# Kernel tuning notes

Hardware: AMD Instinct MI355X
Metric: run time of the kernel (lower is better)

The kernel has to match this reference:

```python
import jax, jax.numpy as jnp
import numpy as np

B, N = 64, 8192
DEPTH, C_IN, C = 12, 4, 128


def _conv1x1(x, W, b):
    # x: [B, Cin, N], W: [Cout, Cin], b: [Cout] -> [B, Cout, N]
    return jnp.einsum('oc,bcn->bon', W, x) + b[None, :, None]


def setup_inputs() -> dict:
    key = jax.random.key(0)
    ks = jax.random.split(key, 10)
    s = 0.05
    return {
        'correspondence': jax.random.normal(ks[0], (B, C_IN, 1, N), jnp.float32),
        'W_first': jax.random.normal(ks[1], (C, C_IN), jnp.float32) * s,
        'b_first': jnp.zeros((C,), jnp.float32),
        'W1s': jax.random.normal(ks[2], (DEPTH, C, C), jnp.float32) * s,
        'b1s': jnp.zeros((DEPTH, C), jnp.float32),
        'W2s': jax.random.normal(ks[3], (DEPTH, C, C), jnp.float32) * s,
        'b2s': jnp.zeros((DEPTH, C), jnp.float32),
        'W_final': jax.random.normal(ks[4], (1, C), jnp.float32) * s,
        'b_final': jnp.zeros((1,), jnp.float32),
    }


def _forward(correspondence, W_first, b_first, W1s, b1s, W2s, b2s, W_final, b_final):
    x_in = correspondence                      # [B, 4, 1, N]
    xc = x_in[:, :, 0, :]                      # [B, 4, N]
    # weightNet: first conv, resnet blocks, final conv (all 1x1)
    h = _conv1x1(xc, W_first, b_first)         # [B, C, N]

    def block(h, p):
        W1, b1, W2, b2 = p
        y = jax.nn.relu(_conv1x1(h, W1, b1))
        y = _conv1x1(y, W2, b2)
        return jax.nn.relu(h + y), None

    h, _ = jax.lax.scan(block, h, (W1s, b1s, W2s, b2s))
    logits = _conv1x1(h, W_final, b_final)[:, 0, :]   # [B, N]
    weight = jax.nn.relu(jnp.tanh(logits))            # [B, N]

    xx = jnp.transpose(xc, (0, 2, 1))                 # [B, N, 4] = [x1, x2, y1, y2]
    x1, x2, y1, y2 = xx[..., 0], xx[..., 1], xx[..., 2], xx[..., 3]
    ones = jnp.ones_like(x1)
    # X: [B, N, 9] epipolar monomials
    X = jnp.stack([y1 * x1, y1 * x2, y1,
                   y2 * x1, y2 * x2, y2,
                   x1, x2, ones], axis=-1)
    # weighted normal matrix per sample: [B, 9, 9]
    XwX = jnp.einsum('bni,bn,bnj->bij', X, weight, X)
    # batched symmetric eigendecomposition; eigh sorts ascending -> min eigvec at index 0
    _, evecs = jnp.linalg.eigh(XwX)
    v = evecs[:, :, 0]                                # [B, 9]
    essential = v / jnp.linalg.norm(v, axis=1, keepdims=True)
    return essential


def reference(correspondence, W_first, b_first, W1s, b1s, W2s, b2s, W_final, b_final):
    return _forward(correspondence, W_first, b_first, W1s, b1s, W2s, b2s, W_final, b_final)
```

## Files before the change

kernel.cpp:

```cpp
#include <hip/hip_runtime.h>
#include <math.h>

#define NPTS 8192
#define CHN 128
#define NLAYER 12
#define LDH 136

typedef __attribute__((ext_vector_type(8))) _Float16 f16x8;
typedef __attribute__((ext_vector_type(4))) float f32x4;

__device__ inline void split_f16(float x, _Float16* hi, _Float16* lo) {
  _Float16 h = (_Float16)x;
  *hi = h;
  *lo = (_Float16)(x - (float)h);
}

union U2h { unsigned int u; _Float16 f[2]; };
union U4h { uint2 u; _Float16 f[4]; };

__global__ void prep_w_kernel(const float* __restrict__ W1s,
                              const float* __restrict__ W2s,
                              _Float16* __restrict__ Whi,
                              _Float16* __restrict__ Wlo) {
  int idx = blockIdx.x * 256 + threadIdx.x;
  if (idx >= 24 * 128 * 128) return;
  int conv = idx >> 14;
  int r = idx & 16383;
  const float* src = (conv & 1) ? (W2s + ((size_t)(conv >> 1) << 14))
                                : (W1s + ((size_t)(conv >> 1) << 14));
  _Float16 h, l;
  split_f16(src[r], &h, &l);
  Whi[idx] = h;
  Wlo[idx] = l;
}

__global__ __launch_bounds__(512, 6) void mlp_xwx_kernel(
    const float* __restrict__ xc,
    const float* __restrict__ Wfirst,
    const float* __restrict__ bfirst,
    const _Float16* __restrict__ Whi,
    const _Float16* __restrict__ Wlo,
    const float* __restrict__ b1s,
    const float* __restrict__ b2s,
    const float* __restrict__ Wfinal,
    const float* __restrict__ bfinal,
    float* __restrict__ partial) {
  __shared__ __align__(16) _Float16 Hh[64 * LDH];
  __shared__ __align__(16) _Float16 Yh[64 * LDH];
  __shared__ float red[8][64];
  const int tid = threadIdx.x;
  const int lane = tid & 63;
  const int wv = tid >> 6;
  const int l16 = lane & 15;
  const int quad = lane >> 4;
  const int o0 = wv << 4;
  const int b = blockIdx.x >> 7;
  const int n0 = (blockIdx.x & 127) << 6;

  const float* xb = xc + ((size_t)b * 4) * NPTS + n0 + lane;
  const float x1 = xb[0 * NPTS];
  const float x2 = xb[1 * NPTS];
  const float y1 = xb[2 * NPTS];
  const float y2 = xb[3 * NPTS];

  {
    #pragma unroll
    for (int j = 0; j < 16; j += 2) {
      int c = o0 + j;
      float h0 = bfirst[c] + Wfirst[c * 4 + 0] * x1 + Wfirst[c * 4 + 1] * x2 +
                 Wfirst[c * 4 + 2] * y1 + Wfirst[c * 4 + 3] * y2;
      float h1 = bfirst[c + 1] + Wfirst[(c + 1) * 4 + 0] * x1 + Wfirst[(c + 1) * 4 + 1] * x2 +
                 Wfirst[(c + 1) * 4 + 2] * y1 + Wfirst[(c + 1) * 4 + 3] * y2;
      U2h ph;
      ph.f[0] = (_Float16)h0;
      ph.f[1] = (_Float16)h1;
      *(unsigned int*)&Hh[lane * LDH + c] = ph.u;
    }
  }
  __syncthreads();

  const size_t arow = (size_t)(o0 + l16) * CHN + (size_t)quad * 8;

  for (int layer = 0; layer < NLAYER; ++layer) {
    {
      const _Float16* W1h = Whi + ((size_t)(2 * layer) << 14);
      const float* b1 = b1s + layer * CHN;
      f16x8 ah[4];
      #pragma unroll
      for (int kt = 0; kt < 4; ++kt)
        ah[kt] = *(const f16x8*)(W1h + arow + kt * 32);
      f32x4 acc[4];
      #pragma unroll
      for (int r = 0; r < 4; ++r) {
        float bv = b1[o0 + quad * 4 + r];
        #pragma unroll
        for (int nt = 0; nt < 4; ++nt) acc[nt][r] = bv;
      }
      #pragma unroll
      for (int kt = 0; kt < 4; ++kt) {
        #pragma unroll
        for (int nt = 0; nt < 4; ++nt) {
          f16x8 bh = *(const f16x8*)&Hh[(nt * 16 + l16) * LDH + kt * 32 + quad * 8];
          acc[nt] = __builtin_amdgcn_mfma_f32_16x16x32_f16(ah[kt], bh, acc[nt], 0, 0, 0);
        }
      }
      #pragma unroll
      for (int nt = 0; nt < 4; ++nt) {
        int p = nt * 16 + l16;
        int c = o0 + quad * 4;
        U4h ph;
        #pragma unroll
        for (int r = 0; r < 4; ++r)
          ph.f[r] = (_Float16)fmaxf(acc[nt][r], 0.0f);
        *(uint2*)&Yh[p * LDH + c] = ph.u;
      }
    }
    __syncthreads();
    {
      const _Float16* W2h = Whi + ((size_t)(2 * layer + 1) << 14);
      const float* b2 = b2s + layer * CHN;
      f16x8 ah[4];
      #pragma unroll
      for (int kt = 0; kt < 4; ++kt)
        ah[kt] = *(const f16x8*)(W2h + arow + kt * 32);
      f32x4 acc[4];
      #pragma unroll
      for (int r = 0; r < 4; ++r) {
        float bv = b2[o0 + quad * 4 + r];
        #pragma unroll
        for (int nt = 0; nt < 4; ++nt) acc[nt][r] = bv;
      }
      #pragma unroll
      for (int kt = 0; kt < 4; ++kt) {
        #pragma unroll
        for (int nt = 0; nt < 4; ++nt) {
          f16x8 bh = *(const f16x8*)&Yh[(nt * 16 + l16) * LDH + kt * 32 + quad * 8];
          acc[nt] = __builtin_amdgcn_mfma_f32_16x16x32_f16(ah[kt], bh, acc[nt], 0, 0, 0);
        }
      }
      #pragma unroll
      for (int nt = 0; nt < 4; ++nt) {
        int p = nt * 16 + l16;
        int c = o0 + quad * 4;
        U4h oh;
        oh.u = *(const uint2*)&Hh[p * LDH + c];
        U4h ph;
        #pragma unroll
        for (int r = 0; r < 4; ++r) {
          float v = fmaxf((float)oh.f[r] + acc[nt][r], 0.0f);
          ph.f[r] = (_Float16)v;
        }
        *(uint2*)&Hh[p * LDH + c] = ph.u;
      }
    }
    __syncthreads();
  }

  {
    float part = 0.0f;
    #pragma unroll
    for (int j = 0; j < 2; ++j) {
      f16x8 kh = *(const f16x8*)&Hh[lane * LDH + o0 + j * 8];
      #pragma unroll
      for (int e = 0; e < 8; ++e)
        part = fmaf(Wfinal[o0 + j * 8 + e], (float)kh[e], part);
    }
    red[wv][lane] = part;
  }
  __syncthreads();
  if (wv == 0) {
    float logit = bfinal[0];
    #pragma unroll
    for (int g = 0; g < 8; ++g) logit += red[g][lane];
    float wgt = fmaxf(tanhf(logit), 0.0f);
    float X[9] = {y1 * x1, y1 * x2, y1, y2 * x1, y2 * x2, y2, x1, x2, 1.0f};
    int k = 0;
    #pragma unroll
    for (int i = 0; i < 9; ++i) {
      #pragma unroll
      for (int j = i; j < 9; ++j) {
        float v = wgt * X[i] * X[j];
        #pragma unroll
        for (int off = 32; off > 0; off >>= 1) v += __shfl_down(v, off, 64);
        if (lane == 0) partial[(size_t)blockIdx.x * 45 + k] = v;
        ++k;
      }
    }
  }
}

__global__ void reduce_xwx_kernel(const float* __restrict__ partial,
                                  float* __restrict__ xwx) {
#pragma clang fp contract(off)
  int tid = blockIdx.x * 256 + threadIdx.x;
  if (tid >= 64 * 45) return;
  int b = tid / 45;
  int k = tid % 45;
  float s = 0.0f;
  for (int blk = 0; blk < 128; ++blk)
    s += partial[((size_t)b * 128 + blk) * 45 + k];
  xwx[tid] = s;
}

__device__ inline float s_sign(float a, float b) { return (b >= 0.0f) ? fabsf(a) : -fabsf(a); }

__device__ inline float slapy2_(float x, float y) {
#pragma clang fp contract(off)
  float ax = fabsf(x), ay = fabsf(y);
  float w = ax > ay ? ax : ay;
  float z = ax > ay ? ay : ax;
  if (z == 0.0f) return w;
  float t = z / w;
  return w * sqrtf(1.0f + t * t);
}

__device__ inline void slartg_(float f, float g, float* c, float* s, float* r) {
#pragma clang fp contract(off)
  if (g == 0.0f) { *c = 1.0f; *s = 0.0f; *r = f; }
  else if (f == 0.0f) { *c = 0.0f; *s = s_sign(1.0f, g); *r = fabsf(g); }
  else {
    float f1 = fabsf(f);
    float d = sqrtf(f * f + g * g);
    *c = f1 / d;
    *r = s_sign(d, f);
    *s = g / (*r);
  }
}

__device__ void slaev2_(float a, float b, float c, float* rt1, float* rt2,
                        float* cs1, float* sn1) {
#pragma clang fp contract(off)
  float sm = a + c, df = a - c, adf = fabsf(df), tb = b + b, ab = fabsf(tb);
  float acmx, acmn;
  if (fabsf(a) > fabsf(c)) { acmx = a; acmn = c; } else { acmx = c; acmn = a; }
  float rt;
  if (adf > ab) { float t = ab / adf; rt = adf * sqrtf(1.0f + t * t); }
  else if (adf < ab) { float t = adf / ab; rt = ab * sqrtf(1.0f + t * t); }
  else rt = ab * sqrtf(2.0f);
  int sgn1;
  if (sm < 0.0f) { *rt1 = 0.5f * (sm - rt); sgn1 = -1; *rt2 = (acmx / (*rt1)) * acmn - (b / (*rt1)) * b; }
  else if (sm > 0.0f) { *rt1 = 0.5f * (sm + rt); sgn1 = 1; *rt2 = (acmx / (*rt1)) * acmn - (b / (*rt1)) * b; }
  else { *rt1 = 0.5f * rt; *rt2 = -0.5f * rt; sgn1 = 1; }
  float cs; int sgn2;
  if (df >= 0.0f) { cs = df + rt; sgn2 = 1; } else { cs = df - rt; sgn2 = -1; }
  float acs = fabsf(cs);
  if (acs > ab) { float ct = -tb / cs; *sn1 = 1.0f / sqrtf(1.0f + ct * ct); *cs1 = ct * (*sn1); }
  else {
    if (ab == 0.0f) { *cs1 = 1.0f; *sn1 = 0.0f; }
    else { float tn = -cs / tb; *cs1 = 1.0f / sqrtf(1.0f + tn * tn); *sn1 = tn * (*cs1); }
  }
  if (sgn1 == sgn2) { float tn = *cs1; *cs1 = -(*sn1); *sn1 = tn; }
}

__global__ void eigen_kernel(const float* __restrict__ xwx, float* __restrict__ out) {
#pragma clang fp contract(off)
  __shared__ float A[81];
  __shared__ float Z[81];
  __shared__ float d1[10], e1[10], tauv[9], wc[10], wsn[10];
  if (threadIdx.x != 0) return;
  const int b = blockIdx.x;
  const int n = 9;
  {
    int k = 0;
    for (int i = 0; i < 9; ++i)
      for (int j = i; j < 9; ++j, ++k) {
        float v = xwx[b * 45 + k];
        A[i * 9 + j] = v;
        A[j * 9 + i] = v;
      }
  }
  for (int i = 0; i < n - 1; ++i) {
    float alpha = A[(i + 1) * 9 + i];
    float xn2 = 0.0f;
    for (int k2 = i + 2; k2 < n; ++k2) xn2 += A[k2 * 9 + i] * A[k2 * 9 + i];
    float xnorm = sqrtf(xn2);
    float taui;
    if (xnorm == 0.0f) taui = 0.0f;
    else {
      float beta = -s_sign(slapy2_(alpha, xnorm), alpha);
      taui = (beta - alpha) / beta;
      float scl = 1.0f / (alpha - beta);
      for (int k2 = i + 2; k2 < n; ++k2) A[k2 * 9 + i] *= scl;
      alpha = beta;
    }
    e1[i + 1] = alpha;
    if (taui != 0.0f) {
      float w[9];
      for (int r = i + 1; r < n; ++r) {
        float sum = A[r * 9 + (i + 1)];
        for (int k2 = i + 2; k2 < n; ++k2) sum += A[r * 9 + k2] * A[k2 * 9 + i];
        w[r] = taui * sum;
      }
      float wv_ = w[i + 1];
      for (int k2 = i + 2; k2 < n; ++k2) wv_ += w[k2] * A[k2 * 9 + i];
      float alpha2 = -0.5f * taui * wv_;
      for (int r = i + 1; r < n; ++r) w[r] += alpha2 * ((r == i + 1) ? 1.0f : A[r * 9 + i]);
      for (int r = i + 1; r < n; ++r) {
        float vr = (r == i + 1) ? 1.0f : A[r * 9 + i];
        for (int cc = i + 1; cc < n; ++cc) {
          float vc = (cc == i + 1) ? 1.0f : A[cc * 9 + i];
          A[r * 9 + cc] -= vr * w[cc] + w[r] * vc;
        }
      }
    }
    tauv[i] = taui;
  }
  for (int k2 = 0; k2 < n; ++k2) d1[k2 + 1] = A[k2 * 9 + k2];
  for (int i = 0; i < 81; ++i) Z[i] = 0.0f;
  for (int i = 0; i < 9; ++i) Z[i * 9 + i] = 1.0f;
  const float eps = 5.9604645e-08f;
  const float eps2 = eps * eps;
  const float safmin = 1.17549435e-38f;
  const int nmaxit = n * 30;
  int jtot = 0;
  int l1 = 1;
  e1[9] = 0.0f;
  while (l1 <= n) {
    if (l1 > 1) e1[l1 - 1] = 0.0f;
    int m;
    if (l1 <= n - 1) {
      for (m = l1; m <= n - 1; ++m) {
        float tst = fabsf(e1[m]);
        if (tst == 0.0f) break;
        if (tst <= (sqrtf(fabsf(d1[m])) * sqrtf(fabsf(d1[m + 1]))) * eps) { e1[m] = 0.0f; break; }
      }
    } else m = n;
    int l = l1;
    int lsv = l, lend = m, lendsv = lend;
    l1 = m + 1;
    if (lend == l) continue;
    if (fabsf(d1[lend]) < fabsf(d1[l])) { lend = lsv; l = lendsv; }
    if (lend > l) {
      while (true) {
        int mq;
        if (l != lend) {
          for (mq = l; mq <= lend - 1; ++mq) {
            float tst = e1[mq] * e1[mq];
            if (tst <= (eps2 * fabsf(d1[mq])) * fabsf(d1[mq + 1]) + safmin) break;
          }
        } else mq = lend;
        if (mq < lend) e1[mq] = 0.0f;
        float p = d1[l];
        if (mq == l) { d1[l] = p; ++l; if (l <= lend) continue; break; }
        if (mq == l + 1) {
          float rt1, rt2, cq, sq;
          slaev2_(d1[l], e1[l], d1[l + 1], &rt1, &rt2, &cq, &sq);
          for (int i = 0; i < 9; ++i) {
            float t = Z[i * 9 + l];
            Z[i * 9 + l] = cq * t - sq * Z[i * 9 + l - 1];
            Z[i * 9 + l - 1] = sq * t + cq * Z[i * 9 + l - 1];
          }
          d1[l] = rt1; d1[l + 1] = rt2; e1[l] = 0.0f;
          l += 2;
          if (l <= lend) continue;
          break;
        }
        if (jtot == nmaxit) break;
        ++jtot;
        float g = (d1[l + 1] - p) / (2.0f * e1[l]);
        float r = slapy2_(g, 1.0f);
        g = d1[mq] - p + e1[l] / (g + s_sign(r, g));
        float sq = 1.0f, cq = 1.0f;
        p = 0.0f;
        for (int i = mq - 1; i >= l; --i) {
          float f = sq * e1[i];
          float bq = cq * e1[i];
          slartg_(g, f, &cq, &sq, &r);
          if (i != mq - 1) e1[i + 1] = r;
          g = d1[i + 1] - p;
          r = (d1[i] - g) * sq + 2.0f * cq * bq;
          p = sq * r;
          d1[i + 1] = g + p;
          g = cq * r - bq;
          wc[i] = cq;
          wsn[i] = -sq;
        }
        for (int jj = mq - 1; jj >= l; --jj) {
          float cj = wc[jj], sj = wsn[jj];
          for (int i = 0; i < 9; ++i) {
            float t = Z[i * 9 + jj];
            Z[i * 9 + jj] = cj * t - sj * Z[i * 9 + jj - 1];
            Z[i * 9 + jj - 1] = sj * t + cj * Z[i * 9 + jj - 1];
          }
        }
        d1[l] -= p;
        e1[l] = g;
      }
    } else {
      while (true) {
        int mq;
        if (l != lend) {
          for (mq = l; mq >= lend + 1; --mq) {
            float tst = e1[mq - 1] * e1[mq - 1];
            if (tst <= (eps2 * fabsf(d1[mq])) * fabsf(d1[mq - 1]) + safmin) break;
          }
        } else mq = lend;
        if (mq > lend) e1[mq - 1] = 0.0f;
        float p = d1[l];
        if (mq == l) { d1[l] = p; --l; if (l >= lend) continue; break; }
        if (mq == l - 1) {
          float rt1, rt2, cq, sq;
          slaev2_(d1[l - 1], e1[l - 1], d1[l], &rt1, &rt2, &cq, &sq);
          for (int i = 0; i < 9; ++i) {
            float t = Z[i * 9 + l - 1];
            Z[i * 9 + l - 1] = cq * t - sq * Z[i * 9 + l - 2];
            Z[i * 9 + l - 2] = sq * t + cq * Z[i * 9 + l - 2];
          }
          d1[l - 1] = rt1; d1[l] = rt2; e1[l - 1] = 0.0f;
          l -= 2;
          if (l >= lend) continue;
          break;
        }
        if (jtot == nmaxit) break;
        ++jtot;
        float g = (d1[l - 1] - p) / (2.0f * e1[l - 1]);
        float r = slapy2_(g, 1.0f);
        g = d1[mq] - p + e1[l - 1] / (g + s_sign(r, g));
        float sq = 1.0f, cq = 1.0f;
        p = 0.0f;
        for (int i = mq; i <= l - 1; ++i) {
          float f = sq * e1[i];
          float bq = cq * e1[i];
          slartg_(g, f, &cq, &sq, &r);
          if (i != mq) e1[i - 1] = r;
          g = d1[i] - p;
          r = (d1[i + 1] - g) * sq + 2.0f * cq * bq;
          p = sq * r;
          d1[i] = g + p;
          g = cq * r - bq;
          wc[i] = cq;
          wsn[i] = sq;
        }
        for (int jj = mq; jj <= l - 1; ++jj) {
          float cj = wc[jj], sj = wsn[jj];
          for (int i = 0; i < 9; ++i) {
            float t = Z[i * 9 + jj];
            Z[i * 9 + jj] = cj * t - sj * Z[i * 9 + jj - 1];
            Z[i * 9 + jj - 1] = sj * t + cj * Z[i * 9 + jj - 1];
          }
        }
        d1[l] -= p;
        e1[l - 1] = g;
      }
    }
  }
  for (int ii = 2; ii <= n; ++ii) {
    int i = ii - 1, k = i;
    float p = d1[i];
    for (int j = ii; j <= n; ++j)
      if (d1[j] < p) { k = j; p = d1[j]; }
    if (k != i) {
      d1[k] = d1[i];
      d1[i] = p;
      for (int r = 0; r < 9; ++r) {
        float t = Z[r * 9 + (i - 1)];
        Z[r * 9 + (i - 1)] = Z[r * 9 + (k - 1)];
        Z[r * 9 + (k - 1)] = t;
      }
    }
  }
  float z0[9];
  for (int i = 0; i < 9; ++i) z0[i] = Z[i * 9 + 0];
  for (int i = n - 2; i >= 0; --i) {
    float taui = tauv[i];
    if (taui == 0.0f) continue;
    float sum = z0[i + 1];
    for (int k2 = i + 2; k2 < n; ++k2) sum += A[k2 * 9 + i] * z0[k2];
    sum *= taui;
    z0[i + 1] -= sum;
    for (int k2 = i + 2; k2 < n; ++k2) z0[k2] -= A[k2 * 9 + i] * sum;
  }
  float nrm = 0.0f;
  for (int i = 0; i < 9; ++i) nrm += z0[i] * z0[i];
  float q = sqrtf(nrm);
  for (int i = 0; i < 9; ++i) out[b * 9 + i] = z0[i] / q;
}

extern "C" void kernel_launch(void* const* d_in, const int* in_sizes, int n_in,
                              void* d_out, int out_size, void* d_ws, size_t ws_size,
                              hipStream_t stream) {
  const float* xc     = (const float*)d_in[0];
  const float* Wfirst = (const float*)d_in[1];
  const float* bfirst = (const float*)d_in[2];
  const float* W1s    = (const float*)d_in[3];
  const float* b1s    = (const float*)d_in[4];
  const float* W2s    = (const float*)d_in[5];
  const float* b2s    = (const float*)d_in[6];
  const float* Wfinal = (const float*)d_in[7];
  const float* bfinal = (const float*)d_in[8];

  _Float16* Whi = (_Float16*)d_ws;
  _Float16* Wlo = Whi + (size_t)24 * 128 * 128;
  float* partial = (float*)(Wlo + (size_t)24 * 128 * 128);
  float* xwx = partial + (size_t)8192 * 45;

  prep_w_kernel<<<(24 * 128 * 128 + 255) / 256, 256, 0, stream>>>(W1s, W2s, Whi, Wlo);
  mlp_xwx_kernel<<<8192, 512, 0, stream>>>(xc, Wfirst, bfirst, Whi, Wlo, b1s, b2s,
                                           Wfinal, bfinal, partial);
  reduce_xwx_kernel<<<(64 * 45 + 255) / 256, 256, 0, stream>>>(partial, xwx);
  eigen_kernel<<<64, 64, 0, stream>>>(xwx, (float*)d_out);
}
```

Baseline: 952.1 us.

## Give each wave two 16-row output tiles and halve block size to 256 threads

Each wave now computes 32 output channels (two M tiles) instead of 16, so the block shrinks from 8 waves to 4. Every LDS B-fragment load now feeds two MFMAs, which halves LDS read traffic per MFMA and halves the number of waves taking part in each barrier. The cost is twice the accumulator and A-fragment registers per wave and fewer waves per block available to hide latency. Launch bounds change to (256, 4).

```diff
diff --git a/kernel.cpp b/kernel.cpp
--- a/kernel.cpp
+++ b/kernel.cpp
@@ -34,7 +34,7 @@
   Wlo[idx] = l;
 }
 
-__global__ __launch_bounds__(512, 6) void mlp_xwx_kernel(
+__global__ __launch_bounds__(256, 4) void mlp_xwx_kernel(
     const float* __restrict__ xc,
     const float* __restrict__ Wfirst,
     const float* __restrict__ bfirst,
@@ -47,13 +47,13 @@
     float* __restrict__ partial) {
   __shared__ __align__(16) _Float16 Hh[64 * LDH];
   __shared__ __align__(16) _Float16 Yh[64 * LDH];
-  __shared__ float red[8][64];
+  __shared__ float red[4][64];
   const int tid = threadIdx.x;
   const int lane = tid & 63;
   const int wv = tid >> 6;
   const int l16 = lane & 15;
   const int quad = lane >> 4;
-  const int o0 = wv << 4;
+  const int o0 = wv << 5;
   const int b = blockIdx.x >> 7;
   const int n0 = (blockIdx.x & 127) << 6;
 
@@ -65,7 +65,7 @@
 
   {
     #pragma unroll
-    for (int j = 0; j < 16; j += 2) {
+    for (int j = 0; j < 32; j += 2) {
       int c = o0 + j;
       float h0 = bfirst[c] + Wfirst[c * 4 + 0] * x1 + Wfirst[c * 4 + 1] * x2 +
                  Wfirst[c * 4 + 2] * y1 + Wfirst[c * 4 + 3] * y2;
@@ -85,73 +85,89 @@
     {
       const _Float16* W1h = Whi + ((size_t)(2 * layer) << 14);
       const float* b1 = b1s + layer * CHN;
-      f16x8 ah[4];
-      #pragma unroll
-      for (int kt = 0; kt < 4; ++kt)
-        ah[kt] = *(const f16x8*)(W1h + arow + kt * 32);
-      f32x4 acc[4];
-      #pragma unroll
-      for (int r = 0; r < 4; ++r) {
-        float bv = b1[o0 + quad * 4 + r];
-        #pragma unroll
-        for (int nt = 0; nt < 4; ++nt) acc[nt][r] = bv;
-      }
+      f16x8 ah[2][4];
+      #pragma unroll
+      for (int mt = 0; mt < 2; ++mt)
+        #pragma unroll
+        for (int kt = 0; kt < 4; ++kt)
+          ah[mt][kt] = *(const f16x8*)(W1h + arow + (size_t)mt * 16 * CHN + kt * 32);
+      f32x4 acc[2][4];
+      #pragma unroll
+      for (int mt = 0; mt < 2; ++mt)
+        #pragma unroll
+        for (int r = 0; r < 4; ++r) {
+          float bv = b1[o0 + mt * 16 + quad * 4 + r];
+          #pragma unroll
+          for (int nt = 0; nt < 4; ++nt) acc[mt][nt][r] = bv;
+        }
       #pragma unroll
       for (int kt = 0; kt < 4; ++kt) {
         #pragma unroll
         for (int nt = 0; nt < 4; ++nt) {
           f16x8 bh = *(const f16x8*)&Hh[(nt * 16 + l16) * LDH + kt * 32 + quad * 8];
-          acc[nt] = __builtin_amdgcn_mfma_f32_16x16x32_f16(ah[kt], bh, acc[nt], 0, 0, 0);
-        }
-      }
-      #pragma unroll
-      for (int nt = 0; nt < 4; ++nt) {
-        int p = nt * 16 + l16;
-        int c = o0 + quad * 4;
-        U4h ph;
-        #pragma unroll
-        for (int r = 0; r < 4; ++r)
-          ph.f[r] = (_Float16)fmaxf(acc[nt][r], 0.0f);
-        *(uint2*)&Yh[p * LDH + c] = ph.u;
-      }
+          #pragma unroll
+          for (int mt = 0; mt < 2; ++mt)
+            acc[mt][nt] = __builtin_amdgcn_mfma_f32_16x16x32_f16(ah[mt][kt], bh, acc[mt][nt], 0, 0, 0);
+        }
+      }
+      #pragma unroll
+      for (int mt = 0; mt < 2; ++mt)
+        #pragma unroll
+        for (int nt = 0; nt < 4; ++nt) {
+          int p = nt * 16 + l16;
+          int c = o0 + mt * 16 + quad * 4;
+          U4h ph;
+          #pragma unroll
+          for (int r = 0; r < 4; ++r)
+            ph.f[r] = (_Float16)fmaxf(acc[mt][nt][r], 0.0f);
+          *(uint2*)&Yh[p * LDH + c] = ph.u;
+        }
     }
     __syncthreads();
     {
       const _Float16* W2h = Whi + ((size_t)(2 * layer + 1) << 14);
       const float* b2 = b2s + layer * CHN;
-      f16x8 ah[4];
-      #pragma unroll
-      for (int kt = 0; kt < 4; ++kt)
-        ah[kt] = *(const f16x8*)(W2h + arow + kt * 32);
-      f32x4 acc[4];
-      #pragma unroll
-      for (int r = 0; r < 4; ++r) {
-        float bv = b2[o0 + quad * 4 + r];
-        #pragma unroll
-        for (int nt = 0; nt < 4; ++nt) acc[nt][r] = bv;
-      }
+      f16x8 ah[2][4];
+      #pragma unroll
+      for (int mt = 0; mt < 2; ++mt)
+        #pragma unroll
+        for (int kt = 0; kt < 4; ++kt)
+          ah[mt][kt] = *(const f16x8*)(W2h + arow + (size_t)mt * 16 * CHN + kt * 32);
+      f32x4 acc[2][4];
+      #pragma unroll
+      for (int mt = 0; mt < 2; ++mt)
+        #pragma unroll
+        for (int r = 0; r < 4; ++r) {
+          float bv = b2[o0 + mt * 16 + quad * 4 + r];
+          #pragma unroll
+          for (int nt = 0; nt < 4; ++nt) acc[mt][nt][r] = bv;
+        }
       #pragma unroll
       for (int kt = 0; kt < 4; ++kt) {
         #pragma unroll
         for (int nt = 0; nt < 4; ++nt) {
           f16x8 bh = *(const f16x8*)&Yh[(nt * 16 + l16) * LDH + kt * 32 + quad * 8];
-          acc[nt] = __builtin_amdgcn_mfma_f32_16x16x32_f16(ah[kt], bh, acc[nt], 0, 0, 0);
-        }
-      }
-      #pragma unroll
-      for (int nt = 0; nt < 4; ++nt) {
-        int p = nt * 16 + l16;
-        int c = o0 + quad * 4;
-        U4h oh;
-        oh.u = *(const uint2*)&Hh[p * LDH + c];
-        U4h ph;
-        #pragma unroll
-        for (int r = 0; r < 4; ++r) {
-          float v = fmaxf((float)oh.f[r] + acc[nt][r], 0.0f);
-          ph.f[r] = (_Float16)v;
-        }
-        *(uint2*)&Hh[p * LDH + c] = ph.u;
-      }
+          #pragma unroll
+          for (int mt = 0; mt < 2; ++mt)
+            acc[mt][nt] = __builtin_amdgcn_mfma_f32_16x16x32_f16(ah[mt][kt], bh, acc[mt][nt], 0, 0, 0);
+        }
+      }
+      #pragma unroll
+      for (int mt = 0; mt < 2; ++mt)
+        #pragma unroll
+        for (int nt = 0; nt < 4; ++nt) {
+          int p = nt * 16 + l16;
+          int c = o0 + mt * 16 + quad * 4;
+          U4h oh;
+          oh.u = *(const uint2*)&Hh[p * LDH + c];
+          U4h ph;
+          #pragma unroll
+          for (int r = 0; r < 4; ++r) {
+            float v = fmaxf((float)oh.f[r] + acc[mt][nt][r], 0.0f);
+            ph.f[r] = (_Float16)v;
+          }
+          *(uint2*)&Hh[p * LDH + c] = ph.u;
+        }
     }
     __syncthreads();
   }
@@ -159,7 +175,7 @@
   {
     float part = 0.0f;
     #pragma unroll
-    for (int j = 0; j < 2; ++j) {
+    for (int j = 0; j < 4; ++j) {
       f16x8 kh = *(const f16x8*)&Hh[lane * LDH + o0 + j * 8];
       #pragma unroll
       for (int e = 0; e < 8; ++e)
@@ -169,9 +185,7 @@
   }
   __syncthreads();
   if (wv == 0) {
-    float logit = bfinal[0];
-    #pragma unroll
-    for (int g = 0; g < 8; ++g) logit += red[g][lane];
+    float logit = red[0][lane] + red[1][lane] + red[2][lane] + red[3][lane] + bfinal[0];
     float wgt = fmaxf(tanhf(logit), 0.0f);
     float X[9] = {y1 * x1, y1 * x2, y1, y2 * x1, y2 * x2, y2, x1, x2, 1.0f};
     int k = 0;
@@ -495,7 +509,7 @@
   float* xwx = partial + (size_t)8192 * 45;
 
   prep_w_kernel<<<(24 * 128 * 128 + 255) / 256, 256, 0, stream>>>(W1s, W2s, Whi, Wlo);
-  mlp_xwx_kernel<<<8192, 512, 0, stream>>>(xc, Wfirst, bfirst, Whi, Wlo, b1s, b2s,
+  mlp_xwx_kernel<<<8192, 256, 0, stream>>>(xc, Wfirst, bfirst, Whi, Wlo, b1s, b2s,
                                            Wfinal, bfinal, partial);
   reduce_xwx_kernel<<<(64 * 45 + 255) / 256, 256, 0, stream>>>(partial, xwx);
   eigen_kernel<<<64, 64, 0, stream>>>(xwx, (float*)d_out);
```

Result: no change. 953.3 us (+0.1%).
